# Performance work log

Measured on AMD Instinct MI355X. Metric: run time of the kernel, lower is better.

The kernel has to match this reference:

```python
import jax, jax.numpy as jnp
import numpy as np

EPS = 1e-12  # matches F.normalize default eps

def _angle(e):
    # e: [N, D] embeddings
    d = e[:, None, :] - e[None, :, :]                      # [N, N, D] pairwise differences
    n = jnp.linalg.norm(d, axis=-1, keepdims=True)         # [N, N, 1]
    d = d / jnp.maximum(n, EPS)                            # normalized diffs; diagonal stays 0
    # all-triplet cosines: for each anchor i, Gram matrix of its normalized diffs
    return jnp.einsum('ijd,ikd->ijk', d, d)                # [N, N, N]

def _smooth_l1_mean(a, b):
    # torch F.smooth_l1_loss with beta=1.0, reduction='mean'
    x = jnp.abs(a - b)
    return jnp.mean(jnp.where(x < 1.0, 0.5 * x * x, x - 0.5))

def setup_inputs() -> dict:
    key = jax.random.key(0)
    k1, k2 = jax.random.split(key)
    student = jax.random.normal(k1, (384, 256), dtype=jnp.float32)
    teacher = jax.random.normal(k2, (384, 256), dtype=jnp.float32)
    return {"student": student, "teacher": teacher}

def reference(student, teacher):
    s_angle = _angle(student)
    t_angle = _angle(teacher)
    return _smooth_l1_mean(s_angle, t_angle)
```

## Files before the change

### kernel.cpp

```cpp
#include <hip/hip_runtime.h>
#include <hip/hip_bf16.h>

#define NPTS 384
#define NN (NPTS * NPTS)
#define DIMS 256
#define KSPLIT 4
#define KCH (DIMS / KSPLIT)
#define IT 8
#define NZI (NPTS / IT)

__global__ __launch_bounds__(256, 4) void gram_part_kernel(
        const float* __restrict__ Es, const float* __restrict__ Et,
        float* __restrict__ P) {
    const int m  = blockIdx.z >> 2;
    const int kc = (blockIdx.z & 3) * KCH;
    const float* __restrict__ E = m ? Et : Es;
    float* __restrict__ Gp = P + (size_t)blockIdx.z * NN;

    const int tx = threadIdx.x;
    const int ty = threadIdx.y;
    const int i  = blockIdx.x * 32 + 2 * ty;
    const int j  = blockIdx.y * 32 + 2 * tx;

    const float4* __restrict__ a0 = (const float4*)(E + i * DIMS + kc);
    const float4* __restrict__ a1 = (const float4*)(E + (i + 1) * DIMS + kc);
    const float4* __restrict__ b0 = (const float4*)(E + j * DIMS + kc);
    const float4* __restrict__ b1 = (const float4*)(E + (j + 1) * DIMS + kc);

    float g00 = 0.f, g01 = 0.f, g10 = 0.f, g11 = 0.f;
#pragma unroll
    for (int k = 0; k < KCH / 4; k++) {
        const float4 av0 = a0[k], av1 = a1[k], bv0 = b0[k], bv1 = b1[k];
        g00 = fmaf(av0.x, bv0.x, g00); g00 = fmaf(av0.y, bv0.y, g00);
        g00 = fmaf(av0.z, bv0.z, g00); g00 = fmaf(av0.w, bv0.w, g00);
        g01 = fmaf(av0.x, bv1.x, g01); g01 = fmaf(av0.y, bv1.y, g01);
        g01 = fmaf(av0.z, bv1.z, g01); g01 = fmaf(av0.w, bv1.w, g01);
        g10 = fmaf(av1.x, bv0.x, g10); g10 = fmaf(av1.y, bv0.y, g10);
        g10 = fmaf(av1.z, bv0.z, g10); g10 = fmaf(av1.w, bv0.w, g10);
        g11 = fmaf(av1.x, bv1.x, g11); g11 = fmaf(av1.y, bv1.y, g11);
        g11 = fmaf(av1.z, bv1.z, g11); g11 = fmaf(av1.w, bv1.w, g11);
    }

    *(float2*)(Gp + i * NPTS + j)       = make_float2(g00, g01);
    *(float2*)(Gp + (i + 1) * NPTS + j) = make_float2(g10, g11);
}

__global__ __launch_bounds__(256, 4) void derive_kernel(
        const float* __restrict__ P,
        float* __restrict__ Gs, float* __restrict__ Gt,
        float2* __restrict__ UHs, float2* __restrict__ UHt,
        float* __restrict__ out) {
    const int idx = blockIdx.x * 256 + threadIdx.x;
    if (idx == 0) out[0] = 0.0f;
    const int z   = idx / NN;
    const int rem = idx - z * NN;
    const int i   = rem / NPTS;
    const int j   = rem - i * NPTS;

    const float* __restrict__ bz = P + (size_t)z * 4 * NN;
    const int di = i * (NPTS + 1);
    const int dj = j * (NPTS + 1);

    const float g   = bz[rem] + bz[NN + rem] + bz[2 * NN + rem] + bz[3 * NN + rem];
    const float gii = bz[di]  + bz[NN + di]  + bz[2 * NN + di]  + bz[3 * NN + di];
    const float gjj = bz[dj]  + bz[NN + dj]  + bz[2 * NN + dj]  + bz[3 * NN + dj];

    const float v = gii + gjj - 2.0f * g;
    const float n = sqrtf(fmaxf(v, 0.0f));
    const float u = (i == j) ? 0.0f : (1.0f / fmaxf(n, 1e-12f));

    (z ? Gt : Gs)[rem]   = g;
    (z ? UHt : UHs)[rem] = make_float2(u, 0.5f * gii - g);
}

__global__ __launch_bounds__(256, 3) void rkd_main_kernel(
        const float* __restrict__ Gs, const float* __restrict__ Gt,
        const float2* __restrict__ UHs, const float2* __restrict__ UHt,
        float* __restrict__ out) {
    const int tlin = blockIdx.x;
    const int kt = (int)((sqrtf(8.0f * (float)tlin + 1.0f) - 1.0f) * 0.5f);
    const int jt = tlin - (kt * (kt + 1)) / 2;

    const int tx = threadIdx.x;
    const int ty = threadIdx.y;
    const int jb = jt * 64 + 4 * ty;
    const int kb = kt * 64 + 4 * tx;
    const int ibase = blockIdx.y * IT;

    float gs[4][4], gt[4][4];
#pragma unroll
    for (int a = 0; a < 4; a++) {
        const float4 vs = *(const float4*)(Gs + (jb + a) * NPTS + kb);
        const float4 vt = *(const float4*)(Gt + (jb + a) * NPTS + kb);
        gs[a][0] = vs.x; gs[a][1] = vs.y; gs[a][2] = vs.z; gs[a][3] = vs.w;
        gt[a][0] = vt.x; gt[a][1] = vt.y; gt[a][2] = vt.z; gt[a][3] = vt.w;
    }

    const float4* __restrict__ pjs = (const float4*)(UHs + (size_t)ibase * NPTS + jb);
    const float4* __restrict__ pjt = (const float4*)(UHt + (size_t)ibase * NPTS + jb);
    const float4* __restrict__ pks = (const float4*)(UHs + (size_t)ibase * NPTS + kb);
    const float4* __restrict__ pkt = (const float4*)(UHt + (size_t)ibase * NPTS + kb);

    const bool offd = (jt != kt);
    float wh[4][4];
#pragma unroll
    for (int a = 0; a < 4; a++)
#pragma unroll
        for (int b = 0; b < 4; b++) {
            const int jj = jb + a, kk = kb + b;
            wh[a][b] = (kk > jj) ? 1.0f : ((kk == jj) ? 0.5f : 0.0f);
        }

    float4 L[8];
    L[0] = pjs[0]; L[1] = pjs[1];
    L[2] = pjt[0]; L[3] = pjt[1];
    L[4] = pks[0]; L[5] = pks[1];
    L[6] = pkt[0]; L[7] = pkt[1];

    float acc = 0.0f;
#pragma unroll 2
    for (int iz = 0; iz < IT; iz++) {
        const int nz = (iz + 1 < IT) ? iz + 1 : iz;
        const int ro = nz * (NPTS / 2);
        float4 Ln[8];
        Ln[0] = pjs[ro];     Ln[1] = pjs[ro + 1];
        Ln[2] = pjt[ro];     Ln[3] = pjt[ro + 1];
        Ln[4] = pks[ro];     Ln[5] = pks[ro + 1];
        Ln[6] = pkt[ro];     Ln[7] = pkt[ro + 1];

        const float u_sj[4] = {L[0].x, L[0].z, L[1].x, L[1].z};
        const float h_sj[4] = {L[0].y, L[0].w, L[1].y, L[1].w};
        const float u_tj[4] = {L[2].x, L[2].z, L[3].x, L[3].z};
        const float h_tj[4] = {L[2].y, L[2].w, L[3].y, L[3].w};
        const float u_sk[4] = {L[4].x, L[4].z, L[5].x, L[5].z};
        const float h_sk[4] = {L[4].y, L[4].w, L[5].y, L[5].w};
        const float u_tk[4] = {L[6].x, L[6].z, L[7].x, L[7].z};
        const float h_tk[4] = {L[6].y, L[6].w, L[7].y, L[7].w};

        if (offd) {
#pragma unroll
            for (int a = 0; a < 4; a++) {
                const float usa = u_sj[a], hsa = h_sj[a];
                const float uta = u_tj[a], hta = h_tj[a];
#pragma unroll
                for (int b = 0; b < 4; b++) {
                    const float ts = gs[a][b] + hsa + h_sk[b];
                    const float tt = gt[a][b] + hta + h_tk[b];
                    const float ps = usa * u_sk[b];
                    const float pt = uta * u_tk[b];
                    const float mt = pt * tt;
                    const float d  = fmaf(ps, ts, -mt);
                    const float q  = d * d;
                    const float w  = fmaf(2.0f, fabsf(d), -1.0f);
                    acc += __builtin_amdgcn_fmed3f(q, w, 1.0f);
                }
            }
        } else {
#pragma unroll
            for (int a = 0; a < 4; a++) {
                const float usa = u_sj[a], hsa = h_sj[a];
                const float uta = u_tj[a], hta = h_tj[a];
#pragma unroll
                for (int b = 0; b < 4; b++) {
                    const float ts = gs[a][b] + hsa + h_sk[b];
                    const float tt = gt[a][b] + hta + h_tk[b];
                    const float ps = usa * u_sk[b];
                    const float pt = uta * u_tk[b];
                    const float mt = pt * tt;
                    const float d  = fmaf(ps, ts, -mt);
                    const float q  = d * d;
                    const float w  = fmaf(2.0f, fabsf(d), -1.0f);
                    const float l  = __builtin_amdgcn_fmed3f(q, w, 1.0f);
                    acc = fmaf(wh[a][b], l, acc);
                }
            }
        }

#pragma unroll
        for (int r = 0; r < 8; r++) L[r] = Ln[r];
    }

#pragma unroll
    for (int off = 32; off > 0; off >>= 1)
        acc += __shfl_down(acc, off, 64);

    __shared__ float wsum[4];
    const int tid  = ty * 16 + tx;
    const int wid  = tid >> 6;
    const int lane = tid & 63;
    if (lane == 0) wsum[wid] = acc;
    __syncthreads();
    if (tid == 0) {
        const float s = wsum[0] + wsum[1] + wsum[2] + wsum[3];
        atomicAdd(out, s * (1.0f / (384.0f * 384.0f * 384.0f)));
    }
}

extern "C" void kernel_launch(void* const* d_in, const int* in_sizes, int n_in,
                              void* d_out, int out_size, void* d_ws, size_t ws_size,
                              hipStream_t stream) {
    const float* student = (const float*)d_in[0];
    const float* teacher = (const float*)d_in[1];
    float* out = (float*)d_out;

    float*  P   = (float*)d_ws;
    float*  Gs  = P + 8 * NN;
    float*  Gt  = Gs + NN;
    float2* UHs = (float2*)(Gt + NN);
    float2* UHt = UHs + NN;

    gram_part_kernel<<<dim3(NPTS / 32, NPTS / 32, 8), dim3(16, 16), 0, stream>>>(
        student, teacher, P);

    derive_kernel<<<dim3(2 * NN / 256), 256, 0, stream>>>(
        P, Gs, Gt, UHs, UHt, out);

    rkd_main_kernel<<<dim3(21, NZI), dim3(16, 16), 0, stream>>>(
        Gs, Gt, UHs, UHt, out);
}
```

Baseline: 109.2 us.

## Fuse split-K Gram partials and derive step into one block-reduced kernel

Replaces the split-K Gram kernel and the separate derive kernel with one kernel. Each 1024-thread block computes four K-chunk partials, reduces them in shared memory, and directly writes G and the (u,h) pairs. Row squared norms are computed in-block instead of read from the Gram diagonal. This removes the large partial-sum workspace traffic and one kernel launch. The cost is fewer, larger blocks with a sync, and slight numerical differences from using separately computed norms.

```diff
diff --git a/kernel.cpp b/kernel.cpp
--- a/kernel.cpp
+++ b/kernel.cpp
@@ -4,32 +4,59 @@
 #define NPTS 384
 #define NN (NPTS * NPTS)
 #define DIMS 256
-#define KSPLIT 4
-#define KCH (DIMS / KSPLIT)
 #define IT 8
 #define NZI (NPTS / IT)
 
-__global__ __launch_bounds__(256, 4) void gram_part_kernel(
+__global__ __launch_bounds__(1024) void gram_fused_kernel(
         const float* __restrict__ Es, const float* __restrict__ Et,
-        float* __restrict__ P) {
-    const int m  = blockIdx.z >> 2;
-    const int kc = (blockIdx.z & 3) * KCH;
-    const float* __restrict__ E = m ? Et : Es;
-    float* __restrict__ Gp = P + (size_t)blockIdx.z * NN;
+        float* __restrict__ Gs, float* __restrict__ Gt,
+        float2* __restrict__ UHs, float2* __restrict__ UHt,
+        float* __restrict__ out) {
+    const int z = blockIdx.z;
+    const float* __restrict__ E  = z ? Et : Es;
+    float*       __restrict__ G  = z ? Gt : Gs;
+    float2*      __restrict__ UH = z ? UHt : UHs;
 
     const int tx = threadIdx.x;
     const int ty = threadIdx.y;
-    const int i  = blockIdx.x * 32 + 2 * ty;
-    const int j  = blockIdx.y * 32 + 2 * tx;
-
-    const float4* __restrict__ a0 = (const float4*)(E + i * DIMS + kc);
-    const float4* __restrict__ a1 = (const float4*)(E + (i + 1) * DIMS + kc);
-    const float4* __restrict__ b0 = (const float4*)(E + j * DIMS + kc);
-    const float4* __restrict__ b1 = (const float4*)(E + (j + 1) * DIMS + kc);
+    const int kc = threadIdx.z;
+    const int t  = kc * 256 + ty * 16 + tx;
+    const int i0 = blockIdx.x * 32;
+    const int j0 = blockIdx.y * 32;
+
+    if (blockIdx.x == 0 && blockIdx.y == 0 && z == 0 && t == 0) out[0] = 0.0f;
+
+    __shared__ float sn[64];
+    __shared__ float red[4][1024];
+
+    {
+        const int r = t >> 4;
+        const int p = t & 15;
+        const int row = (r < 32) ? (i0 + r) : (j0 + r - 32);
+        const float4* __restrict__ src = (const float4*)(E + row * DIMS) + p * 4;
+        float s = 0.f;
+#pragma unroll
+        for (int q = 0; q < 4; q++) {
+            const float4 v = src[q];
+            s += v.x * v.x + v.y * v.y + v.z * v.z + v.w * v.w;
+        }
+        s += __shfl_xor(s, 1, 64);
+        s += __shfl_xor(s, 2, 64);
+        s += __shfl_xor(s, 4, 64);
+        s += __shfl_xor(s, 8, 64);
+        if (p == 0) sn[r] = s;
+    }
+
+    const int i = i0 + 2 * ty;
+    const int j = j0 + 2 * tx;
+    const float4* __restrict__ a0 = (const float4*)(E + i * DIMS + kc * 64);
+    const float4* __restrict__ a1 = (const float4*)(E + (i + 1) * DIMS + kc * 64);
+    const float4* __restrict__ b0 = (const float4*)(E + j * DIMS + kc * 64);
+    const float4* __restrict__ b1 = (const float4*)(E + (j + 1) * DIMS + kc * 64);
 
     float g00 = 0.f, g01 = 0.f, g10 = 0.f, g11 = 0.f;
-#pragma unroll
-    for (int k = 0; k < KCH / 4; k++) {
+#pragma unroll 4
+    for (int k = 0; k < 16; k++) {
         const float4 av0 = a0[k], av1 = a1[k], bv0 = b0[k], bv1 = b1[k];
         g00 = fmaf(av0.x, bv0.x, g00); g00 = fmaf(av0.y, bv0.y, g00);
         g00 = fmaf(av0.z, bv0.z, g00); g00 = fmaf(av0.w, bv0.w, g00);
@@ -41,36 +68,37 @@
         g11 = fmaf(av1.z, bv1.z, g11); g11 = fmaf(av1.w, bv1.w, g11);
     }
 
-    *(float2*)(Gp + i * NPTS + j)       = make_float2(g00, g01);
-    *(float2*)(Gp + (i + 1) * NPTS + j) = make_float2(g10, g11);
-}
-
-__global__ __launch_bounds__(256, 4) void derive_kernel(
-        const float* __restrict__ P,
-        float* __restrict__ Gs, float* __restrict__ Gt,
-        float2* __restrict__ UHs, float2* __restrict__ UHt,
-        float* __restrict__ out) {
-    const int idx = blockIdx.x * 256 + threadIdx.x;
-    if (idx == 0) out[0] = 0.0f;
-    const int z   = idx / NN;
-    const int rem = idx - z * NN;
-    const int i   = rem / NPTS;
-    const int j   = rem - i * NPTS;
-
-    const float* __restrict__ bz = P + (size_t)z * 4 * NN;
-    const int di = i * (NPTS + 1);
-    const int dj = j * (NPTS + 1);
-
-    const float g   = bz[rem] + bz[NN + rem] + bz[2 * NN + rem] + bz[3 * NN + rem];
-    const float gii = bz[di]  + bz[NN + di]  + bz[2 * NN + di]  + bz[3 * NN + di];
-    const float gjj = bz[dj]  + bz[NN + dj]  + bz[2 * NN + dj]  + bz[3 * NN + dj];
-
-    const float v = gii + gjj - 2.0f * g;
-    const float n = sqrtf(fmaxf(v, 0.0f));
-    const float u = (i == j) ? 0.0f : (1.0f / fmaxf(n, 1e-12f));
-
-    (z ? Gt : Gs)[rem]   = g;
-    (z ? UHt : UHs)[rem] = make_float2(u, 0.5f * gii - g);
+    const int t2 = ty * 16 + tx;
+    *(float4*)&red[kc][t2 * 4] = make_float4(g00, g01, g10, g11);
+    __syncthreads();
+
+    if (kc == 0) {
+        const float4 r0 = *(const float4*)&red[0][t2 * 4];
+        const float4 r1 = *(const float4*)&red[1][t2 * 4];
+        const float4 r2 = *(const float4*)&red[2][t2 * 4];
+        const float4 r3 = *(const float4*)&red[3][t2 * 4];
+        const float g[2][2] = {{r0.x + r1.x + r2.x + r3.x, r0.y + r1.y + r2.y + r3.y},
+                               {r0.z + r1.z + r2.z + r3.z, r0.w + r1.w + r2.w + r3.w}};
+        const float si[2] = {sn[2 * ty], sn[2 * ty + 1]};
+        const float sj[2] = {sn[32 + 2 * tx], sn[32 + 2 * tx + 1]};
+
+#pragma unroll
+        for (int r = 0; r < 2; r++) {
+            const int ii = i + r;
+            float uh[4];
+#pragma unroll
+            for (int c = 0; c < 2; c++) {
+                const int jj = j + c;
+                const float gv = g[r][c];
+                const float v  = si[r] + sj[c] - 2.0f * gv;
+                const float n  = sqrtf(fmaxf(v, 0.0f));
+                uh[2 * c]     = (ii == jj) ? 0.0f : (1.0f / fmaxf(n, 1e-12f));
+                uh[2 * c + 1] = 0.5f * si[r] - gv;
+            }
+            *(float2*)(G + ii * NPTS + j) = make_float2(g[r][0], g[r][1]);
+            *(float4*)(UH + ii * NPTS + j) = make_float4(uh[0], uh[1], uh[2], uh[3]);
+        }
+    }
 }
 
 __global__ __launch_bounds__(256, 3) void rkd_main_kernel(
@@ -203,17 +231,13 @@
     const float* teacher = (const float*)d_in[1];
     float* out = (float*)d_out;
 
-    float*  P   = (float*)d_ws;
-    float*  Gs  = P + 8 * NN;
+    float*  Gs  = (float*)d_ws;
     float*  Gt  = Gs + NN;
     float2* UHs = (float2*)(Gt + NN);
     float2* UHt = UHs + NN;
 
-    gram_part_kernel<<<dim3(NPTS / 32, NPTS / 32, 8), dim3(16, 16), 0, stream>>>(
-        student, teacher, P);
-
-    derive_kernel<<<dim3(2 * NN / 256), 256, 0, stream>>>(
-        P, Gs, Gt, UHs, UHt, out);
+    gram_fused_kernel<<<dim3(NPTS / 32, NPTS / 32, 2), dim3(16, 16, 4), 0, stream>>>(
+        student, teacher, Gs, Gt, UHs, UHt, out);
 
     rkd_main_kernel<<<dim3(21, NZI), dim3(16, 16), 0, stream>>>(
         Gs, Gt, UHs, UHt, out);
```

After: 114.5 us. +4.8%, slower.
